# Kernel optimization log

Hardware: AMD Instinct MI355X
Metric: run time of the kernel (lower is better)

Reference implementation:

```python
import jax, jax.numpy as jnp
import numpy as np

T = 4096          # batch_size (time points)
C = 4096          # input_dims[1] == num_filters (channels/neurons)
FW = 64           # filter_width (temporal taps)


def setup_inputs() -> dict:
    key = jax.random.key(0)
    k1, k2, k3 = jax.random.split(key, 3)
    inputs = jax.random.normal(k1, (T, C), dtype=jnp.float32)
    weights = jax.random.uniform(k2, (FW, C), dtype=jnp.float32)
    biases = jax.random.normal(k3, (C,), dtype=jnp.float32) * 0.01
    return {"inputs": inputs, "weights": weights, "biases": biases}


def reference(inputs, weights, biases):
    # weight-norm (normalize_weights=1): per-filter L2 over taps, floored at 1e-8
    wnorms = jnp.maximum(jnp.sqrt(jnp.sum(jnp.square(weights), axis=0)), 1e-8)  # [C]
    filt = jnp.maximum(0.0, weights / wnorms)  # pos_constraint clamp, [FW, C]
    # Original does a full conv2d -> [C, T, 1, C] then takes the diagonal over
    # (batch-channel, filter-channel). Mathematically this is a per-channel
    # depthwise temporal SAME conv (cross-correlation, matching tf.nn.conv2d).
    x = inputs.T[None, :, :]            # [1, C, T]  (NCH)
    k = filt.T[:, None, :]              # [C, 1, FW] (OIH), group size 1
    pre = jax.lax.conv_general_dilated(
        x, k, window_strides=(1,), padding="SAME",
        feature_group_count=C,
        dimension_numbers=("NCH", "OIH", "NCH"))  # [1, C, T]
    # bias add; activation 'lin' = identity; ei_mask is None (num_inh=0)
    out = pre[0].T + biases[None, :]    # [T, C]
    return out
```

## Files before the change

kernel.cpp:

```cpp
#include <hip/hip_runtime.h>


#define T_DIM 4096
#define C_DIM 4096
#define PAD_L 31
#define CB    64
#define KTILE 256
#define SUB   32
#define NSUB  (KTILE / SUB)
#define TPG   16

template <bool GUARD>
__device__ __forceinline__ void fir_body(const float* __restrict__ x,
                                         const float* __restrict__ w,
                                         const float* __restrict__ bia,
                                         float* __restrict__ out,
                                         float* __restrict__ slab,
                                         int c, int cl, int g, int t0) {
    const float* __restrict__ xp = x + c;

    float wf[TPG];
    float ss = 0.0f;
#pragma unroll
    for (int j = 0; j < TPG; ++j) {
        wf[j] = w[(g * TPG + j) * C_DIM + c];
        ss = fmaf(wf[j], wf[j], ss);
    }
    slab[g * CB + cl] = ss;
    __syncthreads();
    ss = slab[0 * CB + cl] + slab[1 * CB + cl] + slab[2 * CB + cl] + slab[3 * CB + cl];
    __syncthreads();
    const float inv = 1.0f / fmaxf(sqrtf(ss), 1e-8f);
#pragma unroll
    for (int j = 0; j < TPG; ++j) wf[j] = fmaxf(wf[j] * inv, 0.0f);

    const float bv = bia[c];

    const int bas = t0 - PAD_L + TPG * g;

#define LOADX(m) ((!GUARD || ((unsigned)(m) < (unsigned)T_DIM))                \
                      ? xp[(long long)(m) * C_DIM] : 0.0f)

    float xbuf[TPG];
#pragma unroll
    for (int i = 0; i < TPG; ++i) xbuf[(1 + i) & 15] = LOADX(bas + i);

    float pfA[16], pfB[16];
#pragma unroll
    for (int i = 0; i < 16; ++i) pfA[i] = LOADX(bas + 16 + i);

    float* __restrict__ yslab = slab + g * (SUB * CB) + cl;
    const float* __restrict__ rbase = slab + g * (8 * CB) + cl;

#define FIR_STEP(k, src)                                                      \
    {                                                                         \
        float a0 = 0.0f, a1 = 0.0f;                                           \
        _Pragma("unroll")                                                     \
        for (int j = 0; j < TPG; j += 2) {                                    \
            a0 = fmaf(wf[j],     xbuf[(1 + (k) + j) & 15],     a0);           \
            a1 = fmaf(wf[j + 1], xbuf[(1 + (k) + j + 1) & 15], a1);           \
        }                                                                     \
        yslab[(k) * CB] = a0 + a1;                  \
        xbuf[(1 + (k)) & 15] = src[(k) & 15];                                 \
    }

#pragma unroll 1
    for (int S = 0; S < NSUB; ++S) {
        const int kb = S * SUB;
#pragma unroll
        for (int i = 0; i < 16; ++i) pfB[i] = LOADX(bas + kb + 32 + i);

        FIR_STEP(0,  pfA) FIR_STEP(1,  pfA) FIR_STEP(2,  pfA) FIR_STEP(3,  pfA)
        FIR_STEP(4,  pfA) FIR_STEP(5,  pfA) FIR_STEP(6,  pfA) FIR_STEP(7,  pfA)
        FIR_STEP(8,  pfA) FIR_STEP(9,  pfA) FIR_STEP(10, pfA) FIR_STEP(11, pfA)
        FIR_STEP(12, pfA) FIR_STEP(13, pfA) FIR_STEP(14, pfA) FIR_STEP(15, pfA)

        if (S < NSUB - 1) {
#pragma unroll
            for (int i = 0; i < 16; ++i) pfA[i] = LOADX(bas + kb + 48 + i);
        }

        FIR_STEP(16, pfB) FIR_STEP(17, pfB) FIR_STEP(18, pfB) FIR_STEP(19, pfB)
        FIR_STEP(20, pfB) FIR_STEP(21, pfB) FIR_STEP(22, pfB) FIR_STEP(23, pfB)
        FIR_STEP(24, pfB) FIR_STEP(25, pfB) FIR_STEP(26, pfB) FIR_STEP(27, pfB)
        FIR_STEP(28, pfB) FIR_STEP(29, pfB) FIR_STEP(30, pfB) FIR_STEP(31, pfB)

        __syncthreads();

        float* __restrict__ op = out + ((long long)(t0 + kb + g * 8)) * C_DIM + c;
#pragma unroll
        for (int i = 0; i < 8; ++i) {
            const float r = rbase[0 * (SUB * CB) + i * CB]
                          + rbase[1 * (SUB * CB) + i * CB]
                          + rbase[2 * (SUB * CB) + i * CB]
                          + rbase[3 * (SUB * CB) + i * CB] + bv;
            __builtin_nontemporal_store(r, op + (long long)i * C_DIM);
        }
        __syncthreads();
    }

#undef FIR_STEP
#undef LOADX
}

__global__ __launch_bounds__(256)
__attribute__((amdgpu_waves_per_eu(2, 4)))
void depthwise_fir_kernel(const float* __restrict__ x, const float* __restrict__ w,
                          const float* __restrict__ bia, float* __restrict__ out) {
    __shared__ float slab[4 * SUB * CB];

    const int tid = threadIdx.x;
    const int g   = tid >> 6;
    const int cl  = tid & 63;
    const int c   = blockIdx.x * CB + cl;
    const int t0  = blockIdx.y * KTILE;

    if (blockIdx.y == 0 || blockIdx.y == gridDim.y - 1)
        fir_body<true>(x, w, bia, out, slab, c, cl, g, t0);
    else
        fir_body<false>(x, w, bia, out, slab, c, cl, g, t0);
}

extern "C" void kernel_launch(void* const* d_in, const int* in_sizes, int n_in,
                              void* d_out, int out_size, void* d_ws, size_t ws_size,
                              hipStream_t stream) {
    const float* x = (const float*)d_in[0];
    const float* w = (const float*)d_in[1];
    const float* b = (const float*)d_in[2];
    float* out = (float*)d_out;

    dim3 grid(C_DIM / CB, T_DIM / KTILE);
    dim3 block(256);
    hipLaunchKernelGGL(depthwise_fir_kernel, grid, block, 0, stream, x, w, b, out);
}
```

Baseline: 51.54 us.

## Replace LDS slab reduction with in-wave bpermute systolic tap-group chain

Moves the four tap groups of each channel into the same wavefront (16 channels x 4 groups per wave), so the weight-norm reduction uses xor shuffles and the partial sums are passed group to group through ds_bpermute in a skewed systolic chain instead of shared memory and block barriers. Only group 3 lanes store the finished output, and the time tile is halved to 128 with smaller prefetch buffers. This removes the LDS slab and all __syncthreads, but group 3 now issues stores from only a quarter of the lanes, giving narrower 64-byte store segments, and each step carries a bpermute on a serial dependency.

```diff
diff --git a/kernel.cpp b/kernel.cpp
--- a/kernel.cpp
+++ b/kernel.cpp
@@ -4,121 +4,121 @@
 #define T_DIM 4096
 #define C_DIM 4096
 #define PAD_L 31
+#define TPG   16
+#define KTILE 128
 #define CB    64
-#define KTILE 256
-#define SUB   32
-#define NSUB  (KTILE / SUB)
-#define TPG   16
+#define NPER  (KTILE / 16)
 
 template <bool GUARD>
 __device__ __forceinline__ void fir_body(const float* __restrict__ x,
                                          const float* __restrict__ w,
                                          const float* __restrict__ bia,
                                          float* __restrict__ out,
-                                         float* __restrict__ slab,
-                                         int c, int cl, int g, int t0) {
+                                         int c, int grp, int t0) {
     const float* __restrict__ xp = x + c;
 
     float wf[TPG];
     float ss = 0.0f;
 #pragma unroll
     for (int j = 0; j < TPG; ++j) {
-        wf[j] = w[(g * TPG + j) * C_DIM + c];
+        wf[j] = w[(grp * TPG + j) * C_DIM + c];
         ss = fmaf(wf[j], wf[j], ss);
     }
-    slab[g * CB + cl] = ss;
-    __syncthreads();
-    ss = slab[0 * CB + cl] + slab[1 * CB + cl] + slab[2 * CB + cl] + slab[3 * CB + cl];
-    __syncthreads();
+    ss += __shfl_xor(ss, 16);
+    ss += __shfl_xor(ss, 32);
     const float inv = 1.0f / fmaxf(sqrtf(ss), 1e-8f);
 #pragma unroll
     for (int j = 0; j < TPG; ++j) wf[j] = fmaxf(wf[j] * inv, 0.0f);
 
     const float bv = bia[c];
 
-    const int bas = t0 - PAD_L + TPG * g;
+    const int W0 = t0 - PAD_L + 15 * grp;
 
-#define LOADX(m) ((!GUARD || ((unsigned)(m) < (unsigned)T_DIM))                \
+#define LOADX(m) ((!GUARD || ((unsigned)(m) < (unsigned)T_DIM))               \
                       ? xp[(long long)(m) * C_DIM] : 0.0f)
 
     float xbuf[TPG];
 #pragma unroll
-    for (int i = 0; i < TPG; ++i) xbuf[(1 + i) & 15] = LOADX(bas + i);
+    for (int i = 0; i < TPG; ++i) xbuf[i] = LOADX(W0 + i);
 
-    float pfA[16], pfB[16];
+    float pfA[8], pfB[8];
 #pragma unroll
-    for (int i = 0; i < 16; ++i) pfA[i] = LOADX(bas + 16 + i);
+    for (int i = 0; i < 8; ++i) pfA[i] = LOADX(W0 + 16 + i);
+#pragma unroll
+    for (int i = 0; i < 8; ++i) pfB[i] = LOADX(W0 + 24 + i);
 
-    float* __restrict__ yslab = slab + g * (SUB * CB) + cl;
-    const float* __restrict__ rbase = slab + g * (8 * CB) + cl;
+    float R = 0.0f;
+    const int paddr = (((threadIdx.x & 63) + 48) & 63) << 2;
+    const bool g0 = (grp == 0);
+    const bool g3 = (grp == 3);
+    float* __restrict__ op0 = out + (long long)t0 * C_DIM + c;
 
-#define FIR_STEP(k, src)                                                      \
+#define FIR_STEP(k, src, SGATE)                                               \
     {                                                                         \
         float a0 = 0.0f, a1 = 0.0f;                                           \
         _Pragma("unroll")                                                     \
         for (int j = 0; j < TPG; j += 2) {                                    \
-            a0 = fmaf(wf[j],     xbuf[(1 + (k) + j) & 15],     a0);           \
-            a1 = fmaf(wf[j + 1], xbuf[(1 + (k) + j + 1) & 15], a1);           \
+            a0 = fmaf(wf[j],     xbuf[((k) + j) & 15],     a0);               \
+            a1 = fmaf(wf[j + 1], xbuf[((k) + j + 1) & 15], a1);               \
         }                                                                     \
-        yslab[(k) * CB] = a0 + a1;                  \
-        xbuf[(1 + (k)) & 15] = src[(k) & 15];                                 \
+        const float p1 = a0 + a1;                                             \
+        const float pulled = __int_as_float(                                  \
+            __builtin_amdgcn_ds_bpermute(paddr, __float_as_int(R)));          \
+        R = (g0 ? bv : pulled) + p1;                                          \
+        if ((SGATE) && g3)                                                    \
+            __builtin_nontemporal_store(R,                                    \
+                op0 + (long long)(kb + (k) - 3) * C_DIM);                     \
+        xbuf[(k) & 15] = src[(k) & 7];                                        \
     }
 
+    int kb = 0;
+    FIR_STEP(0, pfA, false) FIR_STEP(1, pfA, false) FIR_STEP(2, pfA, false)
+    FIR_STEP(3, pfA, true)  FIR_STEP(4, pfA, true)  FIR_STEP(5, pfA, true)
+    FIR_STEP(6, pfA, true)  FIR_STEP(7, pfA, true)
+#pragma unroll
+    for (int i = 0; i < 8; ++i) pfA[i] = LOADX(W0 + 32 + i);
+    FIR_STEP(8, pfB, true)  FIR_STEP(9, pfB, true)  FIR_STEP(10, pfB, true)
+    FIR_STEP(11, pfB, true) FIR_STEP(12, pfB, true) FIR_STEP(13, pfB, true)
+    FIR_STEP(14, pfB, true) FIR_STEP(15, pfB, true)
+#pragma unroll
+    for (int i = 0; i < 8; ++i) pfB[i] = LOADX(W0 + 40 + i);
+
 #pragma unroll 1
-    for (int S = 0; S < NSUB; ++S) {
-        const int kb = S * SUB;
+    for (int p = 1; p < NPER; ++p) {
+        kb = p * 16;
+        FIR_STEP(0, pfA, true)  FIR_STEP(1, pfA, true)  FIR_STEP(2, pfA, true)
+        FIR_STEP(3, pfA, true)  FIR_STEP(4, pfA, true)  FIR_STEP(5, pfA, true)
+        FIR_STEP(6, pfA, true)  FIR_STEP(7, pfA, true)
 #pragma unroll
-        for (int i = 0; i < 16; ++i) pfB[i] = LOADX(bas + kb + 32 + i);
+        for (int i = 0; i < 8; ++i) pfA[i] = LOADX(W0 + kb + 32 + i);
+        FIR_STEP(8, pfB, true)  FIR_STEP(9, pfB, true)  FIR_STEP(10, pfB, true)
+        FIR_STEP(11, pfB, true) FIR_STEP(12, pfB, true) FIR_STEP(13, pfB, true)
+        FIR_STEP(14, pfB, true) FIR_STEP(15, pfB, true)
+        if (p < NPER - 1) {
+#pragma unroll
+            for (int i = 0; i < 8; ++i) pfB[i] = LOADX(W0 + kb + 40 + i);
+        }
+    }
 
-        FIR_STEP(0,  pfA) FIR_STEP(1,  pfA) FIR_STEP(2,  pfA) FIR_STEP(3,  pfA)
-        FIR_STEP(4,  pfA) FIR_STEP(5,  pfA) FIR_STEP(6,  pfA) FIR_STEP(7,  pfA)
-        FIR_STEP(8,  pfA) FIR_STEP(9,  pfA) FIR_STEP(10, pfA) FIR_STEP(11, pfA)
-        FIR_STEP(12, pfA) FIR_STEP(13, pfA) FIR_STEP(14, pfA) FIR_STEP(15, pfA)
-
-        if (S < NSUB - 1) {
-#pragma unroll
-            for (int i = 0; i < 16; ++i) pfA[i] = LOADX(bas + kb + 48 + i);
-        }
-
-        FIR_STEP(16, pfB) FIR_STEP(17, pfB) FIR_STEP(18, pfB) FIR_STEP(19, pfB)
-        FIR_STEP(20, pfB) FIR_STEP(21, pfB) FIR_STEP(22, pfB) FIR_STEP(23, pfB)
-        FIR_STEP(24, pfB) FIR_STEP(25, pfB) FIR_STEP(26, pfB) FIR_STEP(27, pfB)
-        FIR_STEP(28, pfB) FIR_STEP(29, pfB) FIR_STEP(30, pfB) FIR_STEP(31, pfB)
-
-        __syncthreads();
-
-        float* __restrict__ op = out + ((long long)(t0 + kb + g * 8)) * C_DIM + c;
-#pragma unroll
-        for (int i = 0; i < 8; ++i) {
-            const float r = rbase[0 * (SUB * CB) + i * CB]
-                          + rbase[1 * (SUB * CB) + i * CB]
-                          + rbase[2 * (SUB * CB) + i * CB]
-                          + rbase[3 * (SUB * CB) + i * CB] + bv;
-            __builtin_nontemporal_store(r, op + (long long)i * C_DIM);
-        }
-        __syncthreads();
-    }
+    kb = KTILE;
+    FIR_STEP(0, pfA, true) FIR_STEP(1, pfA, true) FIR_STEP(2, pfA, true)
 
 #undef FIR_STEP
 #undef LOADX
 }
 
-__global__ __launch_bounds__(256)
-__attribute__((amdgpu_waves_per_eu(2, 4)))
-void depthwise_fir_kernel(const float* __restrict__ x, const float* __restrict__ w,
-                          const float* __restrict__ bia, float* __restrict__ out) {
-    __shared__ float slab[4 * SUB * CB];
-
-    const int tid = threadIdx.x;
-    const int g   = tid >> 6;
-    const int cl  = tid & 63;
-    const int c   = blockIdx.x * CB + cl;
-    const int t0  = blockIdx.y * KTILE;
-
+__global__ __launch_bounds__(256) void depthwise_fir_kernel(
+    const float* __restrict__ x, const float* __restrict__ w,
+    const float* __restrict__ bia, float* __restrict__ out) {
+    const int lane = threadIdx.x & 63;
+    const int wave = threadIdx.x >> 6;
+    const int grp  = lane >> 4;
+    const int c    = blockIdx.x * CB + wave * 16 + (lane & 15);
+    const int t0   = blockIdx.y * KTILE;
     if (blockIdx.y == 0 || blockIdx.y == gridDim.y - 1)
-        fir_body<true>(x, w, bia, out, slab, c, cl, g, t0);
+        fir_body<true>(x, w, bia, out, c, grp, t0);
     else
-        fir_body<false>(x, w, bia, out, slab, c, cl, g, t0);
+        fir_body<false>(x, w, bia, out, c, grp, t0);
 }
 
 extern "C" void kernel_launch(void* const* d_in, const int* in_sizes, int n_in,
```

Result: slower. 56.87 us (+10.3%).
